# Performance work log

Measured on AMD Instinct MI355X. Metric: run time of the kernel, lower is better.

Reference implementation:

```python
import jax, jax.numpy as jnp
import numpy as np
from jax import lax

T, H, L = 4096, 1024, 2  # seq_len, hidden (=input_dim), num_layers


def setup_inputs() -> dict:
    key = jax.random.key(0)
    ks = jax.random.split(key, 12)
    s = 1.0 / np.sqrt(H)
    u = lambda k, shp: jax.random.uniform(k, shp, jnp.float32, -s, s)
    return {
        "x": jax.random.normal(ks[0], (T, 1, H), jnp.float32),
        # encoder LSTM params, stacked over layers: W_ih/W_hh [L,4H,H], biases [L,4H]
        "enc_W_ih": u(ks[1], (L, 4 * H, H)),
        "enc_W_hh": u(ks[2], (L, 4 * H, H)),
        "enc_b_ih": u(ks[3], (L, 4 * H)),
        "enc_b_hh": u(ks[4], (L, 4 * H)),
        # decoder LSTM params
        "dec_W_ih": u(ks[5], (L, 4 * H, H)),
        "dec_W_hh": u(ks[6], (L, 4 * H, H)),
        "dec_b_ih": u(ks[7], (L, 4 * H)),
        "dec_b_hh": u(ks[8], (L, 4 * H)),
        # output Linear: H -> input_dim (=H)
        "out_W": u(ks[9], (H, H)),
        "out_b": u(ks[10], (H,)),
    }


def _lstm_layer(x_seq, W_ih, W_hh, b_ih, b_hh, h0, c0):
    """One LSTM layer over a full sequence. x_seq: [T,1,I]; returns hs [T,1,H], hT, cT [1,H].
    PyTorch gate order: i, f, g, o."""
    # precompute input contributions for all steps (one big GEMM)
    xg = jnp.einsum('tbi,gi->tbg', x_seq, W_ih) + b_ih  # [T,1,4H]

    def step(carry, xg_t):
        h, c = carry
        g = xg_t + h @ W_hh.T + b_hh  # [1,4H]
        i, f, gg, o = jnp.split(g, 4, axis=-1)
        c = jax.nn.sigmoid(f) * c + jax.nn.sigmoid(i) * jnp.tanh(gg)
        h = jax.nn.sigmoid(o) * jnp.tanh(c)
        return (h, c), h

    (hT, cT), hs = lax.scan(step, (h0, c0), xg)
    return hs, hT, cT


def reference(x, enc_W_ih, enc_W_hh, enc_b_ih, enc_b_hh,
              dec_W_ih, dec_W_hh, dec_b_ih, dec_b_hh, out_W, out_b):
    Tn = x.shape[0]
    nH = enc_W_hh.shape[-1]
    nL = enc_W_ih.shape[0]
    z = jnp.zeros((1, nH), x.dtype)

    # ---- encoder: stacked LSTM, layer-sequential (eval mode: no dropout) ----
    seq = x
    enc_h, enc_c = [], []
    for l in range(nL):
        seq, hT, cT = _lstm_layer(seq, enc_W_ih[l], enc_W_hh[l], enc_b_ih[l], enc_b_hh[l], z, z)
        enc_h.append(hT)
        enc_c.append(cT)

    final_hidden = seq[-1:]  # [1,1,H] = encoded_output[-1].unsqueeze(0)

    # ---- decoder: same constant input fed every step; init state = encoder (h,c) ----
    # The torch loop runs the full stacked LSTM one step at a time with constant input x;
    # stacked LSTMs are layer-separable, so we run each layer over all T steps at once.
    dseq = jnp.broadcast_to(final_hidden, (Tn, 1, nH))
    for l in range(nL):
        dseq, _, _ = _lstm_layer(dseq, dec_W_ih[l], dec_W_hh[l], dec_b_ih[l], dec_b_hh[l], enc_h[l], enc_c[l])

    out = jnp.einsum('tbh,oh->tbo', dseq, out_W) + out_b
    out = jnp.where(out > 0, out, 0.01 * out)  # LeakyReLU(0.01)
    reconstructed = jnp.flip(out, axis=0)  # decoded.reverse()
    return reconstructed, final_hidden
```

## Files before the change

kernel.cpp:

```cpp
#include <hip/hip_runtime.h>
#include <stdint.h>


#define T_STEPS 4096
#define H_DIM   1024
#define SLOT_U64 1024
#define SLOT_DW  2048
#define NSLOT   4097
#define M1 0x7E57u
#define M2 0x7E58u
#define PANIC_ITERS (1u<<25)

using u32 = uint32_t;
using u64 = unsigned long long;

static __device__ __forceinline__ float sigf(float x){ return 1.0f/(1.0f+__expf(-x)); }
static __device__ __forceinline__ float tanh_f(float x){
  x = fminf(20.f, fmaxf(-20.f, x));
  float e = __expf(-2.f*x);
  return (1.f-e)/(1.f+e);
}

static __device__ __forceinline__ bool tag_ok(u64 v, u32 magic){
  return ((((u32)(v>>16))&0xFFFFu)==magic) & (((u32)(v>>48))==magic);
}
static __device__ __forceinline__ float untag1(u64 v){
  return __uint_as_float( (((u32)v)&0xFFFFu) | (((u32)(v>>32))<<16) );
}
static __device__ __forceinline__ u64 tag1(u32 magic, float h){
  u32 b=__float_as_uint(h);
  u64 lo = (u64)((magic<<16)|(b&0xFFFFu));
  u64 hi = ((u64)((magic<<16)|(b>>16)))<<32;
  return hi|lo;
}

static __device__ __forceinline__ void poll_h2(const u64* __restrict__ q,
                                               u32 magic, float* dst,
                                               u32* panic){
  u64 v0=0,v1=0; bool ok0=false,ok1=false; u32 it=0;
  for(;;){
    if(!ok0) v0=__hip_atomic_load(q,  __ATOMIC_RELAXED,__HIP_MEMORY_SCOPE_AGENT);
    if(!ok1) v1=__hip_atomic_load(q+1,__ATOMIC_RELAXED,__HIP_MEMORY_SCOPE_AGENT);
    ok0 = ok0 || tag_ok(v0,magic);
    ok1 = ok1 || tag_ok(v1,magic);
    if(ok0 & ok1) break;
    ++it;
    if((it & 255u)==0u){
      if(__hip_atomic_load(panic,__ATOMIC_RELAXED,__HIP_MEMORY_SCOPE_AGENT)==0xDEADBEEFu) break;
      if(it>PANIC_ITERS){ __hip_atomic_store(panic,0xDEADBEEFu,__ATOMIC_RELAXED,__HIP_MEMORY_SCOPE_AGENT); break; }
    }
    __builtin_amdgcn_s_sleep(4);
  }
  dst[0]=untag1(v0);
  dst[1]=untag1(v1);
}

static __device__ __forceinline__ void poll_in2h2(const u64* __restrict__ qa, u32 mA,
                                                  const u64* __restrict__ qb, u32 mB,
                                                  float* da, float* db, u32* panic){
  u64 a0=0,a1=0,b0=0,b1=0; bool oa0=false,oa1=false,ob0=false,ob1=false; u32 it=0;
  for(;;){
    if(!oa0) a0=__hip_atomic_load(qa,  __ATOMIC_RELAXED,__HIP_MEMORY_SCOPE_AGENT);
    if(!oa1) a1=__hip_atomic_load(qa+1,__ATOMIC_RELAXED,__HIP_MEMORY_SCOPE_AGENT);
    if(!ob0) b0=__hip_atomic_load(qb,  __ATOMIC_RELAXED,__HIP_MEMORY_SCOPE_AGENT);
    if(!ob1) b1=__hip_atomic_load(qb+1,__ATOMIC_RELAXED,__HIP_MEMORY_SCOPE_AGENT);
    oa0 = oa0 || tag_ok(a0,mA);
    oa1 = oa1 || tag_ok(a1,mA);
    ob0 = ob0 || tag_ok(b0,mB);
    ob1 = ob1 || tag_ok(b1,mB);
    if(oa0 & oa1 & ob0 & ob1) break;
    ++it;
    if((it & 255u)==0u){
      if(__hip_atomic_load(panic,__ATOMIC_RELAXED,__HIP_MEMORY_SCOPE_AGENT)==0xDEADBEEFu) break;
      if(it>PANIC_ITERS){ __hip_atomic_store(panic,0xDEADBEEFu,__ATOMIC_RELAXED,__HIP_MEMORY_SCOPE_AGENT); break; }
    }
    __builtin_amdgcn_s_sleep(4);
  }
  da[0]=untag1(a0); da[1]=untag1(a1);
  db[0]=untag1(b0); db[1]=untag1(b1);
}

static __device__ __forceinline__ void lstm_scan_body(
    int kb, int tid, float* st, float* gl,
    const float* __restrict__ xin,
    const u64*  __restrict__ instream,
    u64*        __restrict__ own,
    u32 m_in, u32 m_own,
    const float* __restrict__ Wih, const float* __restrict__ Whh,
    const float* __restrict__ bih, const float* __restrict__ bhh,
    const float* __restrict__ c0,
    float*       __restrict__ cout,
    const u64*  __restrict__ h0slot,
    float*       __restrict__ fh_out,
    u32* __restrict__ panic,
    int mode)
{
  const int hr0=kb*8;
  const int w=tid>>6, l=tid&63;
  const int g=w>>1, q=w&1;
  const int grow0=(g<<10)+hr0+(q<<2);
  const int e0 = 2*tid;
  const int fb  = e0 + 4*(e0>>5);
  const int fbH = 1152+fb;
  const int sb  = l*36;

  float wr0[32],wr1[32],wr2[32],wr3[32];
  {
    const float* srcb = (l<32) ? Wih + (size_t)grow0*H_DIM + l*32
                               : Whh + (size_t)grow0*H_DIM + (l-32)*32;
    #pragma unroll
    for(int i=0;i<8;i++){
      float4 a0=*(const float4*)(srcb + i*4);
      float4 a1=*(const float4*)(srcb + 1024 + i*4);
      float4 a2=*(const float4*)(srcb + 2048 + i*4);
      float4 a3=*(const float4*)(srcb + 3072 + i*4);
      wr0[4*i]=a0.x; wr0[4*i+1]=a0.y; wr0[4*i+2]=a0.z; wr0[4*i+3]=a0.w;
      wr1[4*i]=a1.x; wr1[4*i+1]=a1.y; wr1[4*i+2]=a1.z; wr1[4*i+3]=a1.w;
      wr2[4*i]=a2.x; wr2[4*i+1]=a2.y; wr2[4*i+2]=a2.z; wr2[4*i+3]=a2.w;
      wr3[4*i]=a3.x; wr3[4*i+1]=a3.y; wr3[4*i+2]=a3.z; wr3[4*i+3]=a3.w;
    }
  }

  float bI=0,bF=0,bG=0,bO=0,c_st=0.f,h_st=0.f;
  if(tid<8){
    int o=hr0+tid;
    bI=bih[o]       + bhh[o];
    bF=bih[o+1024]  + bhh[o+1024];
    bG=bih[o+2048]  + bhh[o+2048];
    bO=bih[o+3072]  + bhh[o+3072];
    if(c0)     c_st=c0[o];
    if(h0slot) h_st=untag1(h0slot[o]);
    __hip_atomic_store(own+o, tag1(m_own,h_st), __ATOMIC_RELAXED,__HIP_MEMORY_SCOPE_AGENT);
  }
  if(mode==2){
    st[fb]  =untag1(instream[e0]);
    st[fb+1]=untag1(instream[e0+1]);
  }

  for(int t=0;t<T_STEPS;++t){
    if(mode==0){
      float2 xv=*(const float2*)(xin + (size_t)t*H_DIM + e0);
      st[fb]=xv.x; st[fb+1]=xv.y;
      poll_h2(own + (size_t)t*SLOT_U64 + e0, m_own, st+fbH, panic);
    } else if(mode==2){
      poll_h2(own + (size_t)t*SLOT_U64 + e0, m_own, st+fbH, panic);
    } else {
      poll_in2h2(instream + (size_t)(t+1)*SLOT_U64 + e0, m_in,
                 own      + (size_t)t*SLOT_U64     + e0, m_own,
                 st+fb, st+fbH, panic);
    }
    __syncthreads();
    float p0=0.f,p1=0.f,p2=0.f,p3=0.f;
    #pragma unroll
    for(int i=0;i<8;i++){
      float4 s=*(const float4*)(st+sb+i*4);
      p0+=s.x*wr0[4*i]+s.y*wr0[4*i+1]+s.z*wr0[4*i+2]+s.w*wr0[4*i+3];
      p1+=s.x*wr1[4*i]+s.y*wr1[4*i+1]+s.z*wr1[4*i+2]+s.w*wr1[4*i+3];
      p2+=s.x*wr2[4*i]+s.y*wr2[4*i+1]+s.z*wr2[4*i+2]+s.w*wr2[4*i+3];
      p3+=s.x*wr3[4*i]+s.y*wr3[4*i+1]+s.z*wr3[4*i+2]+s.w*wr3[4*i+3];
    }
    #pragma unroll
    for(int off=32;off;off>>=1){
      p0+=__shfl_down(p0,off,64); p1+=__shfl_down(p1,off,64);
      p2+=__shfl_down(p2,off,64); p3+=__shfl_down(p3,off,64);
    }
    if(l==0){ gl[w*4+0]=p0; gl[w*4+1]=p1; gl[w*4+2]=p2; gl[w*4+3]=p3; }
    __syncthreads();
    if(tid<8){
      float gi=bI+gl[tid], gf=bF+gl[8+tid], gg=bG+gl[16+tid], go=bO+gl[24+tid];
      c_st = sigf(gf)*c_st + sigf(gi)*tanh_f(gg);
      h_st = sigf(go)*tanh_f(c_st);
      __hip_atomic_store(own + (size_t)(t+1)*SLOT_U64 + hr0 + tid,
                         tag1(m_own,h_st), __ATOMIC_RELAXED,__HIP_MEMORY_SCOPE_AGENT);
      if(t==T_STEPS-1){
        cout[hr0+tid]=c_st;
        if(fh_out) fh_out[hr0+tid]=h_st;
      }
    }
  }
}

__global__ __launch_bounds__(512,2) void lstm_scan_pair(
    const float* __restrict__ xinA,
    const u64*  __restrict__ insA, u64* __restrict__ ownA, u32 miA, u32 moA,
    const float* __restrict__ WihA, const float* __restrict__ WhhA,
    const float* __restrict__ bihA, const float* __restrict__ bhhA,
    const float* __restrict__ c0A, float* __restrict__ coutA,
    const u64*  __restrict__ h0A, float* __restrict__ fhA, int modeA,
    const u64*  __restrict__ insB, u64* __restrict__ ownB, u32 miB, u32 moB,
    const float* __restrict__ WihB, const float* __restrict__ WhhB,
    const float* __restrict__ bihB, const float* __restrict__ bhhB,
    const float* __restrict__ c0B, float* __restrict__ coutB,
    const u64*  __restrict__ h0B, float* __restrict__ fhB, int modeB,
    u32* __restrict__ panic)
{
  __shared__ __align__(16) float st[2304];
  __shared__ float gl[32];
  const int b=blockIdx.x, tid=threadIdx.x;
  if(b<128){
    lstm_scan_body(b, tid, st, gl, xinA, insA, ownA, miA, moA,
                   WihA, WhhA, bihA, bhhA, c0A, coutA, h0A, fhA, panic, modeA);
  } else {
    lstm_scan_body(b-128, tid, st, gl, nullptr, insB, ownB, miB, moB,
                   WihB, WhhB, bihB, bhhB, c0B, coutB, h0B, fhB, panic, modeB);
  }
}

__global__ __launch_bounds__(256) void proj_out(
    const u64* __restrict__ SB, const float* __restrict__ oW,
    const float* __restrict__ ob, float* __restrict__ out)
{
  __shared__ __align__(16) float hb[1024];
  const int tp=blockIdx.x, tid=threadIdx.x;
  #pragma unroll
  for(int j=0;j<4;j++)
    hb[tid*4+j] = untag1(SB[(size_t)(tp+1)*SLOT_U64 + tid*4 + j]);
  __syncthreads();
  #pragma unroll
  for(int j=0;j<4;j++){
    int o = tid + 256*j;
    const float* wr = oW + (size_t)o*H_DIM;
    float acc=0.f;
    for(int k=0;k<1024;k+=4){
      float4 wv=*(const float4*)(wr+k);
      acc += wv.x*hb[k]+wv.y*hb[k+1]+wv.z*hb[k+2]+wv.w*hb[k+3];
    }
    acc += ob[o];
    acc = acc>0.f ? acc : 0.01f*acc;
    out[(size_t)(4095-tp)*H_DIM + o]=acc;
  }
}

extern "C" void kernel_launch(void* const* d_in, const int* in_sizes, int n_in,
                              void* d_out, int out_size, void* d_ws, size_t ws_size,
                              hipStream_t stream) {
  const float* x    = (const float*)d_in[0];
  const float* eWih = (const float*)d_in[1];
  const float* eWhh = (const float*)d_in[2];
  const float* ebih = (const float*)d_in[3];
  const float* ebhh = (const float*)d_in[4];
  const float* dWih = (const float*)d_in[5];
  const float* dWhh = (const float*)d_in[6];
  const float* dbih = (const float*)d_in[7];
  const float* dbhh = (const float*)d_in[8];
  const float* oW   = (const float*)d_in[9];
  const float* ob   = (const float*)d_in[10];
  float* out = (float*)d_out;
  u32* ws = (u32*)d_ws;

  const size_t REGION = (size_t)NSLOT*SLOT_DW;
  u64*   SA    = (u64*)ws;
  u64*   SB    = (u64*)(ws + REGION);
  float* CA    = (float*)(ws + 2*REGION);
  u32*   panic = ws + 2*REGION + 2048;
  const size_t LSTRIDE = (size_t)4096*1024;

  size_t clr_bytes = (2*REGION + 2048 + 64)*4;
  hipMemsetAsync(d_ws, 0, clr_bytes, stream);

  lstm_scan_pair<<<256,512,0,stream>>>(
      x, nullptr, SA, 0u, M1,
      eWih, eWhh, ebih, ebhh,
      nullptr, CA, nullptr, nullptr, 0,
      SA, SB, M1, M1,
      eWih+LSTRIDE, eWhh+LSTRIDE, ebih+4096, ebhh+4096,
      nullptr, CA+1024, nullptr, out + (size_t)T_STEPS*H_DIM, 1,
      panic);

  lstm_scan_pair<<<256,512,0,stream>>>(
      nullptr, SB + (size_t)4096*SLOT_U64, SA, 0u, M2,
      dWih, dWhh, dbih, dbhh,
      CA, CA, SA + (size_t)4096*SLOT_U64, nullptr, 2,
      SA, SB, M2, M2,
      dWih+LSTRIDE, dWhh+LSTRIDE, dbih+4096, dbhh+4096,
      CA+1024, CA+1024, SB + (size_t)4096*SLOT_U64, nullptr, 3,
      panic);

  proj_out<<<4096,256,0,stream>>>(SB, oW, ob, out);
}
```

Baseline: 25.27 ms.

## Double-buffer scan state, drop second barrier, tile output projection over timesteps

```diff
diff --git a/kernel.cpp b/kernel.cpp
--- a/kernel.cpp
+++ b/kernel.cpp
@@ -9,7 +9,7 @@
 #define NSLOT   4097
 #define M1 0x7E57u
 #define M2 0x7E58u
-#define PANIC_ITERS (1u<<25)
+#define PANIC_ITERS (1u<<23)
 
 using u32 = uint32_t;
 using u64 = unsigned long long;
@@ -44,12 +44,11 @@
     ok0 = ok0 || tag_ok(v0,magic);
     ok1 = ok1 || tag_ok(v1,magic);
     if(ok0 & ok1) break;
-    ++it;
-    if((it & 255u)==0u){
+    if(((++it)&255u)==0u){
       if(__hip_atomic_load(panic,__ATOMIC_RELAXED,__HIP_MEMORY_SCOPE_AGENT)==0xDEADBEEFu) break;
       if(it>PANIC_ITERS){ __hip_atomic_store(panic,0xDEADBEEFu,__ATOMIC_RELAXED,__HIP_MEMORY_SCOPE_AGENT); break; }
-    }
-    __builtin_amdgcn_s_sleep(4);
+      __builtin_amdgcn_s_sleep(1);
+    }
   }
   dst[0]=untag1(v0);
   dst[1]=untag1(v1);
@@ -69,19 +68,18 @@
     ob0 = ob0 || tag_ok(b0,mB);
     ob1 = ob1 || tag_ok(b1,mB);
     if(oa0 & oa1 & ob0 & ob1) break;
-    ++it;
-    if((it & 255u)==0u){
+    if(((++it)&255u)==0u){
       if(__hip_atomic_load(panic,__ATOMIC_RELAXED,__HIP_MEMORY_SCOPE_AGENT)==0xDEADBEEFu) break;
       if(it>PANIC_ITERS){ __hip_atomic_store(panic,0xDEADBEEFu,__ATOMIC_RELAXED,__HIP_MEMORY_SCOPE_AGENT); break; }
-    }
-    __builtin_amdgcn_s_sleep(4);
+      __builtin_amdgcn_s_sleep(1);
+    }
   }
   da[0]=untag1(a0); da[1]=untag1(a1);
   db[0]=untag1(b0); db[1]=untag1(b1);
 }
 
 static __device__ __forceinline__ void lstm_scan_body(
-    int kb, int tid, float* st, float* gl,
+    int kb, int tid, float (*st)[2304],
     const float* __restrict__ xin,
     const u64*  __restrict__ instream,
     u64*        __restrict__ own,
@@ -97,8 +95,7 @@
 {
   const int hr0=kb*8;
   const int w=tid>>6, l=tid&63;
-  const int g=w>>1, q=w&1;
-  const int grow0=(g<<10)+hr0+(q<<2);
+  const int r = hr0 + w;
   const int e0 = 2*tid;
   const int fb  = e0 + 4*(e0>>5);
   const int fbH = 1152+fb;
@@ -106,14 +103,15 @@
 
   float wr0[32],wr1[32],wr2[32],wr3[32];
   {
-    const float* srcb = (l<32) ? Wih + (size_t)grow0*H_DIM + l*32
-                               : Whh + (size_t)grow0*H_DIM + (l-32)*32;
+    const size_t GS = (size_t)1024*1024;
+    const float* srcb = (l<32) ? Wih + (size_t)r*H_DIM + l*32
+                               : Whh + (size_t)r*H_DIM + (l-32)*32;
     #pragma unroll
     for(int i=0;i<8;i++){
       float4 a0=*(const float4*)(srcb + i*4);
-      float4 a1=*(const float4*)(srcb + 1024 + i*4);
-      float4 a2=*(const float4*)(srcb + 2048 + i*4);
-      float4 a3=*(const float4*)(srcb + 3072 + i*4);
+      float4 a1=*(const float4*)(srcb + GS + i*4);
+      float4 a2=*(const float4*)(srcb + 2*GS + i*4);
+      float4 a3=*(const float4*)(srcb + 3*GS + i*4);
       wr0[4*i]=a0.x; wr0[4*i+1]=a0.y; wr0[4*i+2]=a0.z; wr0[4*i+3]=a0.w;
       wr1[4*i]=a1.x; wr1[4*i+1]=a1.y; wr1[4*i+2]=a1.z; wr1[4*i+3]=a1.w;
       wr2[4*i]=a2.x; wr2[4*i+1]=a2.y; wr2[4*i+2]=a2.z; wr2[4*i+3]=a2.w;
@@ -122,38 +120,39 @@
   }
 
   float bI=0,bF=0,bG=0,bO=0,c_st=0.f,h_st=0.f;
-  if(tid<8){
-    int o=hr0+tid;
-    bI=bih[o]       + bhh[o];
-    bF=bih[o+1024]  + bhh[o+1024];
-    bG=bih[o+2048]  + bhh[o+2048];
-    bO=bih[o+3072]  + bhh[o+3072];
-    if(c0)     c_st=c0[o];
-    if(h0slot) h_st=untag1(h0slot[o]);
-    __hip_atomic_store(own+o, tag1(m_own,h_st), __ATOMIC_RELAXED,__HIP_MEMORY_SCOPE_AGENT);
+  if(l==0){
+    bI=bih[r]       + bhh[r];
+    bF=bih[r+1024]  + bhh[r+1024];
+    bG=bih[r+2048]  + bhh[r+2048];
+    bO=bih[r+3072]  + bhh[r+3072];
+    if(c0)     c_st=c0[r];
+    if(h0slot) h_st=untag1(h0slot[r]);
+    __hip_atomic_store(own + r, tag1(m_own,h_st), __ATOMIC_RELAXED,__HIP_MEMORY_SCOPE_AGENT);
   }
   if(mode==2){
-    st[fb]  =untag1(instream[e0]);
-    st[fb+1]=untag1(instream[e0+1]);
+    float v0=untag1(instream[e0]), v1=untag1(instream[e0+1]);
+    st[0][fb]=v0; st[0][fb+1]=v1;
+    st[1][fb]=v0; st[1][fb+1]=v1;
   }
 
   for(int t=0;t<T_STEPS;++t){
+    float* S = st[t&1];
     if(mode==0){
       float2 xv=*(const float2*)(xin + (size_t)t*H_DIM + e0);
-      st[fb]=xv.x; st[fb+1]=xv.y;
-      poll_h2(own + (size_t)t*SLOT_U64 + e0, m_own, st+fbH, panic);
+      poll_h2(own + (size_t)t*SLOT_U64 + e0, m_own, S+fbH, panic);
+      S[fb]=xv.x; S[fb+1]=xv.y;
     } else if(mode==2){
-      poll_h2(own + (size_t)t*SLOT_U64 + e0, m_own, st+fbH, panic);
+      poll_h2(own + (size_t)t*SLOT_U64 + e0, m_own, S+fbH, panic);
     } else {
       poll_in2h2(instream + (size_t)(t+1)*SLOT_U64 + e0, m_in,
                  own      + (size_t)t*SLOT_U64     + e0, m_own,
-                 st+fb, st+fbH, panic);
+                 S+fb, S+fbH, panic);
     }
     __syncthreads();
     float p0=0.f,p1=0.f,p2=0.f,p3=0.f;
     #pragma unroll
     for(int i=0;i<8;i++){
-      float4 s=*(const float4*)(st+sb+i*4);
+      float4 s=*(const float4*)(S+sb+i*4);
       p0+=s.x*wr0[4*i]+s.y*wr0[4*i+1]+s.z*wr0[4*i+2]+s.w*wr0[4*i+3];
       p1+=s.x*wr1[4*i]+s.y*wr1[4*i+1]+s.z*wr1[4*i+2]+s.w*wr1[4*i+3];
       p2+=s.x*wr2[4*i]+s.y*wr2[4*i+1]+s.z*wr2[4*i+2]+s.w*wr2[4*i+3];
@@ -164,17 +163,15 @@
       p0+=__shfl_down(p0,off,64); p1+=__shfl_down(p1,off,64);
       p2+=__shfl_down(p2,off,64); p3+=__shfl_down(p3,off,64);
     }
-    if(l==0){ gl[w*4+0]=p0; gl[w*4+1]=p1; gl[w*4+2]=p2; gl[w*4+3]=p3; }
-    __syncthreads();
-    if(tid<8){
-      float gi=bI+gl[tid], gf=bF+gl[8+tid], gg=bG+gl[16+tid], go=bO+gl[24+tid];
+    if(l==0){
+      float gi=bI+p0, gf=bF+p1, gg=bG+p2, go=bO+p3;
       c_st = sigf(gf)*c_st + sigf(gi)*tanh_f(gg);
       h_st = sigf(go)*tanh_f(c_st);
-      __hip_atomic_store(own + (size_t)(t+1)*SLOT_U64 + hr0 + tid,
+      __hip_atomic_store(own + (size_t)(t+1)*SLOT_U64 + r,
                          tag1(m_own,h_st), __ATOMIC_RELAXED,__HIP_MEMORY_SCOPE_AGENT);
       if(t==T_STEPS-1){
-        cout[hr0+tid]=c_st;
-        if(fh_out) fh_out[hr0+tid]=h_st;
+        cout[r]=c_st;
+        if(fh_out) fh_out[r]=h_st;
       }
     }
   }
@@ -194,40 +191,54 @@
     const u64*  __restrict__ h0B, float* __restrict__ fhB, int modeB,
     u32* __restrict__ panic)
 {
-  __shared__ __align__(16) float st[2304];
-  __shared__ float gl[32];
+  __shared__ __align__(16) float st[2][2304];
   const int b=blockIdx.x, tid=threadIdx.x;
   if(b<128){
-    lstm_scan_body(b, tid, st, gl, xinA, insA, ownA, miA, moA,
+    lstm_scan_body(b, tid, st, xinA, insA, ownA, miA, moA,
                    WihA, WhhA, bihA, bhhA, c0A, coutA, h0A, fhA, panic, modeA);
   } else {
-    lstm_scan_body(b-128, tid, st, gl, nullptr, insB, ownB, miB, moB,
+    lstm_scan_body(b-128, tid, st, nullptr, insB, ownB, miB, moB,
                    WihB, WhhB, bihB, bhhB, c0B, coutB, h0B, fhB, panic, modeB);
   }
 }
 
-__global__ __launch_bounds__(256) void proj_out(
+#define PTILE 16
+__global__ __launch_bounds__(256,2) void proj_out(
     const u64* __restrict__ SB, const float* __restrict__ oW,
     const float* __restrict__ ob, float* __restrict__ out)
 {
-  __shared__ __align__(16) float hb[1024];
-  const int tp=blockIdx.x, tid=threadIdx.x;
-  #pragma unroll
-  for(int j=0;j<4;j++)
-    hb[tid*4+j] = untag1(SB[(size_t)(tp+1)*SLOT_U64 + tid*4 + j]);
+  __shared__ __align__(16) float hb[PTILE][1024];
+  const int tp0=blockIdx.x*PTILE, tid=threadIdx.x;
+  for(int i=0;i<PTILE;i++){
+    u64 v0=SB[(size_t)(tp0+i+1)*SLOT_U64 + tid*4 + 0];
+    u64 v1=SB[(size_t)(tp0+i+1)*SLOT_U64 + tid*4 + 1];
+    u64 v2=SB[(size_t)(tp0+i+1)*SLOT_U64 + tid*4 + 2];
+    u64 v3=SB[(size_t)(tp0+i+1)*SLOT_U64 + tid*4 + 3];
+    float4 f; f.x=untag1(v0); f.y=untag1(v1); f.z=untag1(v2); f.w=untag1(v3);
+    *(float4*)&hb[i][tid*4]=f;
+  }
   __syncthreads();
   #pragma unroll
   for(int j=0;j<4;j++){
     int o = tid + 256*j;
     const float* wr = oW + (size_t)o*H_DIM;
-    float acc=0.f;
+    float acc[PTILE];
+    #pragma unroll
+    for(int i=0;i<PTILE;i++) acc[i]=0.f;
     for(int k=0;k<1024;k+=4){
       float4 wv=*(const float4*)(wr+k);
-      acc += wv.x*hb[k]+wv.y*hb[k+1]+wv.z*hb[k+2]+wv.w*hb[k+3];
-    }
-    acc += ob[o];
-    acc = acc>0.f ? acc : 0.01f*acc;
-    out[(size_t)(4095-tp)*H_DIM + o]=acc;
+      #pragma unroll
+      for(int i=0;i<PTILE;i++){
+        acc[i] += wv.x*hb[i][k]+wv.y*hb[i][k+1]+wv.z*hb[i][k+2]+wv.w*hb[i][k+3];
+      }
+    }
+    float bo=ob[o];
+    #pragma unroll
+    for(int i=0;i<PTILE;i++){
+      float a=acc[i]+bo;
+      a = a>0.f ? a : 0.01f*a;
+      out[(size_t)(4095-(tp0+i))*H_DIM + o]=a;
+    }
   }
 }
 
@@ -276,5 +287,5 @@
       CA+1024, CA+1024, SB + (size_t)4096*SLOT_U64, nullptr, 3,
       panic);
 
-  proj_out<<<4096,256,0,stream>>>(SB, oW, ob, out);
-}
+  proj_out<<<256,256,0,stream>>>(SB, oW, ob, out);
+}
```

After: 38.62 ms. 1.53x slower.
